# Kernel tuning notes

Measured on AMD Instinct MI355X. Metric: run time of the kernel, lower is better.

## Reference

```python
import jax, jax.numpy as jnp
import numpy as np

N_POINTS = 262144
L_LEVELS = 16
FEATS_PER_LEVEL = 2
BASE_RES = 8
FINEST_RES = 512
TABLE_SIZE = 2 ** 12  # log2_hashmap_size = 12
HIDDEN = 256
IN_FEATURES = 3
MLP_IN = L_LEVELS * FEATS_PER_LEVEL + IN_FEATURES - 2  # 33


def _level_params():
    b = np.exp((np.log(FINEST_RES) - np.log(BASE_RES)) / (L_LEVELS - 1))
    res = np.floor(BASE_RES * b ** np.arange(L_LEVELS)).astype(np.int64)
    hsize = np.minimum(res ** 2, TABLE_SIZE)  # per-level hashmap size
    return jnp.asarray(res, jnp.float32), jnp.asarray(hsize, jnp.uint32)


RES, HSIZE = _level_params()
PRIMES = jnp.array([1, 2654435761], dtype=jnp.uint32)  # instant-NGP spatial hash primes (2D)
CORNERS = jnp.array([[0, 0], [0, 1], [1, 0], [1, 1]], dtype=jnp.int32)  # [4,2]


def hash_encode(coords, tables):
    # coords: [N,2] in [0,1]; tables: [L, TABLE_SIZE, F]
    x = coords[None, :, :] * RES[:, None, None]            # [L,N,2] scaled per level
    xi = jnp.floor(x)
    xf = x - xi                                            # fractional part (grad flows to coords)
    inds = xi.astype(jnp.int32)[:, :, None, :] + CORNERS   # [L,N,4,2] corner integer coords
    # bilinear weights: offset 0 -> (1-xf), offset 1 -> xf
    w = jnp.prod(jnp.where(CORNERS == 0, 1.0 - xf[:, :, None, :], xf[:, :, None, :]), axis=-1)  # [L,N,4]
    u = inds.astype(jnp.uint32) * PRIMES                   # [L,N,4,2]
    h = (u[..., 0] ^ u[..., 1]) % HSIZE[:, None, None]     # [L,N,4] hashed table index
    feats = jax.vmap(lambda t, i: t[i])(tables, h)         # [L,N,4,F] gather per level
    out = jnp.einsum('lncf,lnc->lnf', feats, w)            # [L,N,F] bilinear interp
    return jnp.moveaxis(out, 0, 1).reshape(coords.shape[0], -1)  # [N, L*F], level-major per point


def reference(x, tables, W0, b0, W1, b1, W2, b2, W3, b3, W4, b4):
    h = hash_encode(x[:, :2], tables)                      # [N, 32]
    h = jnp.concatenate([h, x[:, 2:]], axis=-1)            # [N, 33]
    h = jax.nn.relu(h @ W0 + b0)
    h = jax.nn.relu(h @ W1 + b1)
    h = jax.nn.relu(h @ W2 + b2)
    h = jax.nn.relu(h @ W3 + b3)
    return h @ W4 + b4                                     # [N, 1]


def setup_inputs() -> dict:
    key = jax.random.key(0)
    ks = jax.random.split(key, 12)

    def lin(kw, fan_in, fan_out):
        s = 1.0 / np.sqrt(fan_in)
        return jax.random.normal(kw, (fan_in, fan_out), jnp.float32) * s

    return {
        'x': jax.random.uniform(ks[0], (N_POINTS, IN_FEATURES), jnp.float32),
        'tables': jax.random.normal(ks[1], (L_LEVELS, TABLE_SIZE, FEATS_PER_LEVEL), jnp.float32) * 1e-2,
        'W0': lin(ks[2], MLP_IN, HIDDEN), 'b0': jnp.zeros((HIDDEN,), jnp.float32),
        'W1': lin(ks[3], HIDDEN, HIDDEN), 'b1': jnp.zeros((HIDDEN,), jnp.float32),
        'W2': lin(ks[4], HIDDEN, HIDDEN), 'b2': jnp.zeros((HIDDEN,), jnp.float32),
        'W3': lin(ks[5], HIDDEN, HIDDEN), 'b3': jnp.zeros((HIDDEN,), jnp.float32),
        'W4': lin(ks[6], HIDDEN, 1),      'b4': jnp.zeros((1,), jnp.float32),
    }
```

## Files before the change

### kernel.cpp

```cpp
#include <hip/hip_runtime.h>
#include <math.h>


typedef __bf16 bf16x8 __attribute__((ext_vector_type(8)));
typedef float  f32x16 __attribute__((ext_vector_type(16)));
typedef unsigned int u32x4 __attribute__((ext_vector_type(4)));
typedef unsigned int u32x2 __attribute__((ext_vector_type(2)));

struct LevelParams {
  float res[16];
  unsigned hsize[16];
  unsigned M[8];
  unsigned c16[8];
  int      sh[8];
};

static constexpr int MTILE = 64;
static constexpr int LDA   = 264;
static constexpr int ACT_ELEMS = MTILE * LDA;
static constexpr int UB_L0 = 0, UB_L1 = 24, UB_L2 = 152, UB_L3 = 280;
static constexpr int UNITS_TOTAL = 408;

__device__ __forceinline__ unsigned short f32_to_bf16_rne(float f) {
  unsigned u = __float_as_uint(f);
  unsigned r = (u + 0x7fffu + ((u >> 16) & 1u)) >> 16;
  return (unsigned short)r;
}
__device__ __forceinline__ float bf16_bits_to_f32(unsigned u16bits) {
  return __uint_as_float(u16bits << 16);
}
__device__ __forceinline__ unsigned pack_hi(unsigned u0, unsigned u1) {
  return (u0 >> 16) | (u1 & 0xffff0000u);
}

__global__ void prep_pack(const float* __restrict__ W0, const float* __restrict__ W1,
                          const float* __restrict__ W2, const float* __restrict__ W3,
                          unsigned short* __restrict__ pack) {
  int b = blockIdx.x;
  int l = threadIdx.x;
  const float* W; int K, s, cq;
  if (b < UB_L1) { W = W0; K = 33; s = b >> 3; cq = b & 7; }
  else {
    int b2 = b - UB_L1; int ly = b2 >> 7; int r = b2 & 127;
    W = (ly == 0) ? W1 : (ly == 1) ? W2 : W3; K = 256; s = r >> 3; cq = r & 7;
  }
  int col = (cq << 5) + (l & 31);
  int kb  = (s << 4) + ((l >> 5) << 3);
  unsigned short* dst = pack + (size_t)b * 1024 + l * 8;
#pragma unroll
  for (int e = 0; e < 8; ++e) {
    int k = kb + e;
    float v = (k < K) ? W[k * 256 + col] : 0.0f;
    unsigned u = __float_as_uint(v);
    unsigned short h = (unsigned short)(u >> 16);
    float hf = bf16_bits_to_f32(u >> 16);
    unsigned short lo = f32_to_bf16_rne(v - hf);
    dst[e]       = h;
    dst[512 + e] = lo;
  }
}

__device__ __forceinline__ void enc_magic(float x0, float x1, const LevelParams& P,
                                          int lvl, const float* __restrict__ tables,
                                          float& o0, float& o1) {
  float rf = P.res[lvl];
  unsigned d = P.hsize[lvl], c = P.c16[lvl], M = P.M[lvl];
  int sh = P.sh[lvl];
  float xs0 = x0 * rf, xs1 = x1 * rf;
  float fl0 = floorf(xs0), fl1 = floorf(xs1);
  float f0 = xs0 - fl0, f1 = xs1 - fl1;
  int i0 = (int)fl0, i1 = (int)fl1;
  unsigned ua0 = (unsigned)i0, ua1 = (unsigned)(i0 + 1);
  unsigned vb0 = (unsigned)i1 * 2654435761u;
  unsigned vb1 = (unsigned)(i1 + 1) * 2654435761u;
  const float* tl = tables + ((size_t)lvl << 13);
  float g0 = 1.0f - f0, g1 = 1.0f - f1;
  unsigned e0 = ua0 ^ vb0, e1 = ua0 ^ vb1, e2 = ua1 ^ vb0, e3 = ua1 ^ vb1;
  unsigned n0 = (e0 >> 16) * c + (e0 & 0xffffu);
  unsigned n1 = (e1 >> 16) * c + (e1 & 0xffffu);
  unsigned n2 = (e2 >> 16) * c + (e2 & 0xffffu);
  unsigned n3 = (e3 >> 16) * c + (e3 & 0xffffu);
  unsigned h0 = n0 - (__umulhi(n0, M) >> sh) * d;
  unsigned h1 = n1 - (__umulhi(n1, M) >> sh) * d;
  unsigned h2 = n2 - (__umulhi(n2, M) >> sh) * d;
  unsigned h3 = n3 - (__umulhi(n3, M) >> sh) * d;
  float a0 = 0.0f, a1 = 0.0f;
  { float w = g0 * g1; a0 += w * tl[2*h0]; a1 += w * tl[2*h0+1]; }
  { float w = g0 * f1; a0 += w * tl[2*h1]; a1 += w * tl[2*h1+1]; }
  { float w = f0 * g1; a0 += w * tl[2*h2]; a1 += w * tl[2*h2+1]; }
  { float w = f0 * f1; a0 += w * tl[2*h3]; a1 += w * tl[2*h3+1]; }
  o0 = a0; o1 = a1;
}
__device__ __forceinline__ void enc_and(float x0, float x1, const LevelParams& P,
                                        int lvl, const float* __restrict__ tables,
                                        float& o0, float& o1) {
  float rf = P.res[lvl];
  float xs0 = x0 * rf, xs1 = x1 * rf;
  float fl0 = floorf(xs0), fl1 = floorf(xs1);
  float f0 = xs0 - fl0, f1 = xs1 - fl1;
  int i0 = (int)fl0, i1 = (int)fl1;
  unsigned ua0 = (unsigned)i0, ua1 = (unsigned)(i0 + 1);
  unsigned vb0 = (unsigned)i1 * 2654435761u;
  unsigned vb1 = (unsigned)(i1 + 1) * 2654435761u;
  const float* tl = tables + ((size_t)lvl << 13);
  float g0 = 1.0f - f0, g1 = 1.0f - f1;
  unsigned h0 = (ua0 ^ vb0) & 4095u, h1 = (ua0 ^ vb1) & 4095u;
  unsigned h2 = (ua1 ^ vb0) & 4095u, h3 = (ua1 ^ vb1) & 4095u;
  float a0 = 0.0f, a1 = 0.0f;
  { float w = g0 * g1; a0 += w * tl[2*h0]; a1 += w * tl[2*h0+1]; }
  { float w = g0 * f1; a0 += w * tl[2*h1]; a1 += w * tl[2*h1+1]; }
  { float w = f0 * g1; a0 += w * tl[2*h2]; a1 += w * tl[2*h2+1]; }
  { float w = f0 * f1; a0 += w * tl[2*h3]; a1 += w * tl[2*h3+1]; }
  o0 = a0; o1 = a1;
}
__device__ __forceinline__ void store_pair(unsigned short* ahi, unsigned short* alo,
                                           int idx, float v0, float v1) {
  unsigned u0 = __float_as_uint(v0), u1 = __float_as_uint(v1);
  float l0 = v0 - __uint_as_float(u0 & 0xffff0000u);
  float l1 = v1 - __uint_as_float(u1 & 0xffff0000u);
  *(unsigned*)(ahi + idx) = pack_hi(u0, u1);
  *(unsigned*)(alo + idx) = pack_hi(__float_as_uint(l0), __float_as_uint(l1));
}

template<int S>
__device__ __forceinline__ void run_layer(unsigned short* __restrict__ ahi,
                                          unsigned short* __restrict__ alo,
                                          const unsigned short* __restrict__ pack,
                                          int ubase,
                                          const float* __restrict__ bias,
                                          int cg, int l) {
  f32x16 acc00 = (f32x16)0.0f, acc01 = (f32x16)0.0f;
  f32x16 acc10 = (f32x16)0.0f, acc11 = (f32x16)0.0f;
  const int i31 = l & 31, p = l >> 5;

  const unsigned short* a0h = ahi + i31 * LDA + (p << 3);
  const unsigned short* a1h = ahi + (32 + i31) * LDA + (p << 3);
  const unsigned short* a0l = alo + i31 * LDA + (p << 3);
  const unsigned short* a1l = alo + (32 + i31) * LDA + (p << 3);
  const unsigned short* wb  = pack + (size_t)(ubase + (cg << 1)) * 1024 + l * 8;

  u32x4 A[3][4];
  u32x4 W[3][4];

#define LOADSTEP(j, st)                                                        \
  do {                                                                         \
    A[j][0] = *(const u32x4*)(a0h + ((st) << 4));                              \
    A[j][1] = *(const u32x4*)(a0l + ((st) << 4));                              \
    A[j][2] = *(const u32x4*)(a1h + ((st) << 4));                              \
    A[j][3] = *(const u32x4*)(a1l + ((st) << 4));                              \
    const unsigned short* wp = wb + (size_t)(st) * 8192;                       \
    W[j][0] = *(const u32x4*)(wp);                                             \
    W[j][1] = *(const u32x4*)(wp + 512);                                       \
    W[j][2] = *(const u32x4*)(wp + 1024);                                      \
    W[j][3] = *(const u32x4*)(wp + 1536);                                      \
  } while (0)

  LOADSTEP(0, 0);
  if (S > 1) LOADSTEP(1, 1);

#pragma unroll
  for (int s = 0; s < S; ++s) {
    if (s + 2 < S) { const int j = (s + 2) % 3; LOADSTEP(j, s + 2); }
    const int sl = s % 3;
    bf16x8 AH0 = __builtin_bit_cast(bf16x8, A[sl][0]);
    bf16x8 AL0 = __builtin_bit_cast(bf16x8, A[sl][1]);
    bf16x8 AH1 = __builtin_bit_cast(bf16x8, A[sl][2]);
    bf16x8 AL1 = __builtin_bit_cast(bf16x8, A[sl][3]);
    bf16x8 Wh0 = __builtin_bit_cast(bf16x8, W[sl][0]);
    bf16x8 Wl0 = __builtin_bit_cast(bf16x8, W[sl][1]);
    bf16x8 Wh1 = __builtin_bit_cast(bf16x8, W[sl][2]);
    bf16x8 Wl1 = __builtin_bit_cast(bf16x8, W[sl][3]);
    acc00 = __builtin_amdgcn_mfma_f32_32x32x16_bf16(Wh0, AH0, acc00, 0, 0, 0);
    acc01 = __builtin_amdgcn_mfma_f32_32x32x16_bf16(Wh1, AH0, acc01, 0, 0, 0);
    acc10 = __builtin_amdgcn_mfma_f32_32x32x16_bf16(Wh0, AH1, acc10, 0, 0, 0);
    acc11 = __builtin_amdgcn_mfma_f32_32x32x16_bf16(Wh1, AH1, acc11, 0, 0, 0);
    acc00 = __builtin_amdgcn_mfma_f32_32x32x16_bf16(Wl0, AH0, acc00, 0, 0, 0);
    acc01 = __builtin_amdgcn_mfma_f32_32x32x16_bf16(Wl1, AH0, acc01, 0, 0, 0);
    acc10 = __builtin_amdgcn_mfma_f32_32x32x16_bf16(Wl0, AH1, acc10, 0, 0, 0);
    acc11 = __builtin_amdgcn_mfma_f32_32x32x16_bf16(Wl1, AH1, acc11, 0, 0, 0);
    acc00 = __builtin_amdgcn_mfma_f32_32x32x16_bf16(Wh0, AL0, acc00, 0, 0, 0);
    acc01 = __builtin_amdgcn_mfma_f32_32x32x16_bf16(Wh1, AL0, acc01, 0, 0, 0);
    acc10 = __builtin_amdgcn_mfma_f32_32x32x16_bf16(Wh0, AL1, acc10, 0, 0, 0);
    acc11 = __builtin_amdgcn_mfma_f32_32x32x16_bf16(Wh1, AL1, acc11, 0, 0, 0);
  }
#undef LOADSTEP
  __syncthreads();

#pragma unroll
  for (int pt = 0; pt < 2; ++pt) {
#pragma unroll
    for (int c = 0; c < 2; ++c) {
      f32x16 Acc = pt ? (c ? acc11 : acc10) : (c ? acc01 : acc00);
      int arow = (pt << 5) + i31;
      int colb = (cg << 6) + (c << 5) + (p << 2);
#pragma unroll
      for (int g = 0; g < 4; ++g) {
        int chb = colb + (g << 3);
        float4 bv = *(const float4*)(bias + chb);
        float v0 = fmaxf(Acc[4 * g + 0] + bv.x, 0.0f);
        float v1 = fmaxf(Acc[4 * g + 1] + bv.y, 0.0f);
        float v2 = fmaxf(Acc[4 * g + 2] + bv.z, 0.0f);
        float v3 = fmaxf(Acc[4 * g + 3] + bv.w, 0.0f);
        unsigned u0 = __float_as_uint(v0), u1 = __float_as_uint(v1);
        unsigned u2 = __float_as_uint(v2), u3 = __float_as_uint(v3);
        u32x2 hw = { pack_hi(u0, u1), pack_hi(u2, u3) };
        float l0 = v0 - __uint_as_float(u0 & 0xffff0000u);
        float l1 = v1 - __uint_as_float(u1 & 0xffff0000u);
        float l2 = v2 - __uint_as_float(u2 & 0xffff0000u);
        float l3 = v3 - __uint_as_float(u3 & 0xffff0000u);
        u32x2 lw = { pack_hi(__float_as_uint(l0), __float_as_uint(l1)),
                     pack_hi(__float_as_uint(l2), __float_as_uint(l3)) };
        int base = arow * LDA + chb;
        *(u32x2*)(ahi + base) = hw;
        *(u32x2*)(alo + base) = lw;
      }
    }
  }
  __syncthreads();
}

__global__ __launch_bounds__(256, 2) void inr_main(
    const float* __restrict__ x, const float* __restrict__ tables,
    const float* __restrict__ b0, const float* __restrict__ b1,
    const float* __restrict__ b2, const float* __restrict__ b3,
    const float* __restrict__ W4, const float* __restrict__ b4,
    const unsigned short* __restrict__ pack, float* __restrict__ out,
    LevelParams P) {
  extern __shared__ char smem[];
  unsigned short* ahi = (unsigned short*)smem;
  unsigned short* alo = ahi + ACT_ELEMS;

  const int tid = threadIdx.x;

  {
    int pl = tid >> 2, q = tid & 3;
    size_t pidx = (size_t)blockIdx.x * MTILE + pl;
    float x0 = x[3 * pidx + 0], x1 = x[3 * pidx + 1], x2 = x[3 * pidx + 2];
    int rowb = pl * LDA;
    float o0, o1;
    enc_magic(x0, x1, P, q,      tables, o0, o1); store_pair(ahi, alo, rowb + 2*q,      o0, o1);
    enc_magic(x0, x1, P, q + 4,  tables, o0, o1); store_pair(ahi, alo, rowb + 8 + 2*q,  o0, o1);
    enc_and  (x0, x1, P, q + 8,  tables, o0, o1); store_pair(ahi, alo, rowb + 16 + 2*q, o0, o1);
    enc_and  (x0, x1, P, q + 12, tables, o0, o1); store_pair(ahi, alo, rowb + 24 + 2*q, o0, o1);
    int base = rowb + 32 + (q << 2);
    if (q == 0) {
      unsigned u0 = __float_as_uint(x2);
      float l0 = x2 - __uint_as_float(u0 & 0xffff0000u);
      u32x2 hw = { u0 >> 16, 0u };
      u32x2 lw = { __float_as_uint(l0) >> 16, 0u };
      *(u32x2*)(ahi + base) = hw;
      *(u32x2*)(alo + base) = lw;
    } else {
      u32x2 z = { 0u, 0u };
      *(u32x2*)(ahi + base) = z;
      *(u32x2*)(alo + base) = z;
    }
  }
  __syncthreads();

  const int l  = tid & 63;
  const int cg = tid >> 6;

  run_layer<3>(ahi, alo, pack, UB_L0, b0, cg, l);
  run_layer<16>(ahi, alo, pack, UB_L1, b1, cg, l);
  run_layer<16>(ahi, alo, pack, UB_L2, b2, cg, l);
  run_layer<16>(ahi, alo, pack, UB_L3, b3, cg, l);

  {
    int pl = tid >> 2, q = tid & 3;
    const unsigned short* hrow = ahi + pl * LDA + (q << 6);
    const unsigned short* lrow = alo + pl * LDA + (q << 6);
    const float* w4p = W4 + (q << 6);
    float sum = 0.0f;
#pragma unroll
    for (int c = 0; c < 8; ++c) {
      u32x4 th = *(const u32x4*)(hrow + (c << 3));
      u32x4 tl = *(const u32x4*)(lrow + (c << 3));
      float4 wA = *(const float4*)(w4p + (c << 3));
      float4 wB = *(const float4*)(w4p + (c << 3) + 4);
#pragma unroll
      for (int u = 0; u < 4; ++u) {
        unsigned hu = th[u], lu = tl[u];
        float v0 = __uint_as_float(hu << 16) + __uint_as_float(lu << 16);
        float v1 = __uint_as_float(hu & 0xffff0000u) + __uint_as_float(lu & 0xffff0000u);
        const float* wp = (u < 2) ? &wA.x : &wB.x;
        int base = (u & 1) << 1;
        sum = fmaf(v0, wp[base], sum);
        sum = fmaf(v1, wp[base + 1], sum);
      }
    }
    sum += __shfl_xor(sum, 1);
    sum += __shfl_xor(sum, 2);
    if (q == 0) out[(size_t)blockIdx.x * MTILE + pl] = sum + b4[0];
  }
}

extern "C" void kernel_launch(void* const* d_in, const int* in_sizes, int n_in,
                              void* d_out, int out_size, void* d_ws, size_t ws_size,
                              hipStream_t stream) {
  const float* x      = (const float*)d_in[0];
  const float* tables = (const float*)d_in[1];
  const float* W0 = (const float*)d_in[2];  const float* b0 = (const float*)d_in[3];
  const float* W1 = (const float*)d_in[4];  const float* b1 = (const float*)d_in[5];
  const float* W2 = (const float*)d_in[6];  const float* b2 = (const float*)d_in[7];
  const float* W3 = (const float*)d_in[8];  const float* b3 = (const float*)d_in[9];
  const float* W4 = (const float*)d_in[10]; const float* b4 = (const float*)d_in[11];
  unsigned short* pack = (unsigned short*)d_ws;
  float* out = (float*)d_out;

  LevelParams P;
  double bgrow = exp((log(512.0) - log(8.0)) / 15.0);
  for (int lvl = 0; lvl < 16; ++lvl) {
    double r = floor(8.0 * pow(bgrow, (double)lvl));
    P.res[lvl] = (float)r;
    double hsd = r * r;
    if (hsd > 4096.0) hsd = 4096.0;
    P.hsize[lvl] = (unsigned)hsd;
  }
  for (int lvl = 0; lvl < 8; ++lvl) {
    unsigned d = P.hsize[lvl];
    P.c16[lvl] = 65536u % d;
    unsigned long long nmax = 65535ULL * d;
    int s = 0;
    while (nmax * d >= (1ULL << (32 + s))) s++;
    P.sh[lvl] = s;
    P.M[lvl] = (unsigned)((1ULL << (32 + s)) / d + 1);
  }

  prep_pack<<<UNITS_TOTAL, 64, 0, stream>>>(W0, W1, W2, W3, pack);

  size_t smem_bytes = (size_t)ACT_ELEMS * 2 * 2;
  hipFuncSetAttribute(reinterpret_cast<const void*>(inr_main),
                      hipFuncAttributeMaxDynamicSharedMemorySize, (int)smem_bytes);

  int nblocks = out_size / MTILE;
  inr_main<<<nblocks, 256, smem_bytes, stream>>>(x, tables, b0, b1, b2, b3, W4, b4,
                                                 pack, out, P);
}
```

Measured before the change: 296.4 us.

## Double the point tile to 128 with 512-thread blocks and schedule MFMA interleaving

Doubles the per-block point tile to 128 rows and launches 512 threads, adding a point-group index so pairs of waves share each weight column group across two 64-row halves. This halves how many blocks re-read the packed weights per point. It also reorders the loads so weights are issued first, and adds sched_group_barrier hints to interleave global and LDS loads with the 12 MFMAs per step. LDS use per block doubles to about 135 KB and launch bounds ask for 512x2, which may lower occupancy.

```diff
diff --git a/kernel.cpp b/kernel.cpp
--- a/kernel.cpp
+++ b/kernel.cpp
@@ -15,7 +15,7 @@
   int      sh[8];
 };
 
-static constexpr int MTILE = 64;
+static constexpr int MTILE = 128;
 static constexpr int LDA   = 264;
 static constexpr int ACT_ELEMS = MTILE * LDA;
 static constexpr int UB_L0 = 0, UB_L1 = 24, UB_L2 = 152, UB_L3 = 280;
@@ -128,15 +128,15 @@
                                           const unsigned short* __restrict__ pack,
                                           int ubase,
                                           const float* __restrict__ bias,
-                                          int cg, int l) {
+                                          int pg, int cg, int l) {
   f32x16 acc00 = (f32x16)0.0f, acc01 = (f32x16)0.0f;
   f32x16 acc10 = (f32x16)0.0f, acc11 = (f32x16)0.0f;
   const int i31 = l & 31, p = l >> 5;
 
-  const unsigned short* a0h = ahi + i31 * LDA + (p << 3);
-  const unsigned short* a1h = ahi + (32 + i31) * LDA + (p << 3);
-  const unsigned short* a0l = alo + i31 * LDA + (p << 3);
-  const unsigned short* a1l = alo + (32 + i31) * LDA + (p << 3);
+  const unsigned short* a0h = ahi + ((pg << 6) + i31) * LDA + (p << 3);
+  const unsigned short* a1h = ahi + ((pg << 6) + 32 + i31) * LDA + (p << 3);
+  const unsigned short* a0l = alo + ((pg << 6) + i31) * LDA + (p << 3);
+  const unsigned short* a1l = alo + ((pg << 6) + 32 + i31) * LDA + (p << 3);
   const unsigned short* wb  = pack + (size_t)(ubase + (cg << 1)) * 1024 + l * 8;
 
   u32x4 A[3][4];
@@ -144,15 +144,15 @@
 
 #define LOADSTEP(j, st)                                                        \
   do {                                                                         \
-    A[j][0] = *(const u32x4*)(a0h + ((st) << 4));                              \
-    A[j][1] = *(const u32x4*)(a0l + ((st) << 4));                              \
-    A[j][2] = *(const u32x4*)(a1h + ((st) << 4));                              \
-    A[j][3] = *(const u32x4*)(a1l + ((st) << 4));                              \
     const unsigned short* wp = wb + (size_t)(st) * 8192;                       \
     W[j][0] = *(const u32x4*)(wp);                                             \
     W[j][1] = *(const u32x4*)(wp + 512);                                       \
     W[j][2] = *(const u32x4*)(wp + 1024);                                      \
     W[j][3] = *(const u32x4*)(wp + 1536);                                      \
+    A[j][0] = *(const u32x4*)(a0h + ((st) << 4));                              \
+    A[j][1] = *(const u32x4*)(a0l + ((st) << 4));                              \
+    A[j][2] = *(const u32x4*)(a1h + ((st) << 4));                              \
+    A[j][3] = *(const u32x4*)(a1l + ((st) << 4));                              \
   } while (0)
 
   LOADSTEP(0, 0);
@@ -160,7 +160,8 @@
 
 #pragma unroll
   for (int s = 0; s < S; ++s) {
-    if (s + 2 < S) { const int j = (s + 2) % 3; LOADSTEP(j, s + 2); }
+    const bool pf = (s + 2 < S);
+    if (pf) { const int j = (s + 2) % 3; LOADSTEP(j, s + 2); }
     const int sl = s % 3;
     bf16x8 AH0 = __builtin_bit_cast(bf16x8, A[sl][0]);
     bf16x8 AL0 = __builtin_bit_cast(bf16x8, A[sl][1]);
@@ -182,6 +183,11 @@
     acc01 = __builtin_amdgcn_mfma_f32_32x32x16_bf16(Wh1, AL0, acc01, 0, 0, 0);
     acc10 = __builtin_amdgcn_mfma_f32_32x32x16_bf16(Wh0, AL1, acc10, 0, 0, 0);
     acc11 = __builtin_amdgcn_mfma_f32_32x32x16_bf16(Wh1, AL1, acc11, 0, 0, 0);
+    if (pf) {
+      __builtin_amdgcn_sched_group_barrier(0x020, 4, 0);
+      __builtin_amdgcn_sched_group_barrier(0x100, 4, 0);
+    }
+    __builtin_amdgcn_sched_group_barrier(0x008, 12, 0);
   }
 #undef LOADSTEP
   __syncthreads();
@@ -191,7 +197,7 @@
 #pragma unroll
     for (int c = 0; c < 2; ++c) {
       f32x16 Acc = pt ? (c ? acc11 : acc10) : (c ? acc01 : acc00);
-      int arow = (pt << 5) + i31;
+      int arow = (pg << 6) + (pt << 5) + i31;
       int colb = (cg << 6) + (c << 5) + (p << 2);
 #pragma unroll
       for (int g = 0; g < 4; ++g) {
@@ -219,7 +225,7 @@
   __syncthreads();
 }
 
-__global__ __launch_bounds__(256, 2) void inr_main(
+__global__ __launch_bounds__(512, 2) void inr_main(
     const float* __restrict__ x, const float* __restrict__ tables,
     const float* __restrict__ b0, const float* __restrict__ b1,
     const float* __restrict__ b2, const float* __restrict__ b3,
@@ -259,12 +265,14 @@
   __syncthreads();
 
   const int l  = tid & 63;
-  const int cg = tid >> 6;
-
-  run_layer<3>(ahi, alo, pack, UB_L0, b0, cg, l);
-  run_layer<16>(ahi, alo, pack, UB_L1, b1, cg, l);
-  run_layer<16>(ahi, alo, pack, UB_L2, b2, cg, l);
-  run_layer<16>(ahi, alo, pack, UB_L3, b3, cg, l);
+  const int w  = tid >> 6;
+  const int pg = w & 1;
+  const int cg = w >> 1;
+
+  run_layer<3>(ahi, alo, pack, UB_L0, b0, pg, cg, l);
+  run_layer<16>(ahi, alo, pack, UB_L1, b1, pg, cg, l);
+  run_layer<16>(ahi, alo, pack, UB_L2, b2, pg, cg, l);
+  run_layer<16>(ahi, alo, pack, UB_L3, b3, pg, cg, l);
 
   {
     int pl = tid >> 2, q = tid & 3;
@@ -334,6 +342,6 @@
                       hipFuncAttributeMaxDynamicSharedMemorySize, (int)smem_bytes);
 
   int nblocks = out_size / MTILE;
-  inr_main<<<nblocks, 256, smem_bytes, stream>>>(x, tables, b0, b1, b2, b3, W4, b4,
+  inr_main<<<nblocks, 512, smem_bytes, stream>>>(x, tables, b0, b1, b2, b3, W4, b4,
                                                  pack, out, P);
 }
```

Result: slower. 328.1 us (+10.7%).
